# Optimization experiments

Measured on AMD Instinct MI355X. Metric: run time of the kernel, lower is better.

## Reference

```python
import jax, jax.numpy as jnp
import numpy as np

nT, nB, H, V = 256, 256, 1024, 32000

def setup_inputs() -> dict:
    key = jax.random.key(0)
    ks = jax.random.split(key, 16)
    s = 0.02
    return {
        "tokens": jax.random.randint(ks[0], (nB,), 0, V),
        "prev_hidden": jax.random.normal(ks[1], (1, nB, H), dtype=jnp.float32),
        "enc_outputs": jax.random.normal(ks[2], (nT, nB, H), dtype=jnp.float32),
        "emb": jax.random.normal(ks[3], (V, H), dtype=jnp.float32) * s,
        "W_i2h": jax.random.normal(ks[4], (H, H), dtype=jnp.float32) * s,
        "W_h2h": jax.random.normal(ks[5], (H, H), dtype=jnp.float32) * s,
        "b_h2h": jnp.zeros((H,), dtype=jnp.float32),
        "w_score": jax.random.normal(ks[6], (H,), dtype=jnp.float32) * s,
        "W_ih": jax.random.normal(ks[7], (3 * H, 2 * H), dtype=jnp.float32) * s,
        "b_ih": jnp.zeros((3 * H,), dtype=jnp.float32),
        "W_hh": jax.random.normal(ks[8], (3 * H, H), dtype=jnp.float32) * s,
        "b_hh": jnp.zeros((3 * H,), dtype=jnp.float32),
        "W_out": jax.random.normal(ks[9], (V, H), dtype=jnp.float32) * s,
        "b_out": jnp.zeros((V,), dtype=jnp.float32),
    }

def reference(tokens, prev_hidden, enc_outputs, emb, W_i2h, W_h2h, b_h2h,
              w_score, W_ih, b_ih, W_hh, b_hh, W_out, b_out):
    h0 = prev_hidden[0]                                     # [nB,H]
    cur_emb = emb[tokens]                                   # [nB,H] (dropout = identity at inference)
    # additive (Bahdanau) attention energies
    enc_proj = jnp.einsum('tbh,oh->tbo', enc_outputs, W_i2h)  # [nT,nB,H]
    h_proj = h0 @ W_h2h.T + b_h2h                           # [nB,H]
    e = jnp.einsum('tbh,h->tb', jnp.tanh(enc_proj + h_proj[None]), w_score)  # [nT,nB]
    alpha = jax.nn.softmax(e.T, axis=1)                     # [nB,nT], softmax over time
    context = jnp.einsum('bt,tbh->bh', alpha, enc_outputs)  # [nB,H]
    x = jnp.concatenate([context, cur_emb], axis=1)         # [nB,2H]
    # single GRU step (PyTorch gate order: r, z, n)
    gi = x @ W_ih.T + b_ih                                  # [nB,3H]
    gh = h0 @ W_hh.T + b_hh                                 # [nB,3H]
    hs = h0.shape[-1]
    r = jax.nn.sigmoid(gi[:, :hs] + gh[:, :hs])
    z = jax.nn.sigmoid(gi[:, hs:2*hs] + gh[:, hs:2*hs])
    n = jnp.tanh(gi[:, 2*hs:] + r * gh[:, 2*hs:])
    h_new = (1.0 - z) * n + z * h0                          # [nB,H]
    out = jax.nn.log_softmax(h_new @ W_out.T + b_out, axis=1)  # [nB,V]
    return out, h_new[None], alpha
```

## Files before the change

kernel.cpp:

```cpp
#include <hip/hip_runtime.h>
#include <hip/hip_bf16.h>

typedef __attribute__((ext_vector_type(8))) short bf16x8;
typedef __attribute__((ext_vector_type(4))) float f32x4;
typedef __attribute__((ext_vector_type(4))) int i32x4;
typedef __attribute__((ext_vector_type(4))) unsigned short u16x4;
typedef __attribute__((ext_vector_type(8))) unsigned short u16x8;

#define LDS_STRIDE 72

__device__ __forceinline__ unsigned short f2bf(float f) {
    __hip_bfloat16 h = __float2bfloat16(f);
    unsigned short u; __builtin_memcpy(&u, &h, 2); return u;
}
__device__ __forceinline__ float bf2f(unsigned short u) {
    union { unsigned u; float f; } v; v.u = ((unsigned)u) << 16; return v.f;
}
__device__ __forceinline__ float fast_sigmoid(float x) { return 1.f / (1.f + __expf(-x)); }
__device__ __forceinline__ float fast_tanh(float x)    { return 1.f - 2.f / (__expf(2.f * x) + 1.f); }

#define GLOAD_LDS16(gp, lp) __builtin_amdgcn_global_load_lds( \
    (const __attribute__((address_space(1))) void*)(gp), \
    (__attribute__((address_space(3))) void*)(lp), 16, 0, 0)


#define STA(LB, HF, PTR) do { \
    GLOAD_LDS16((PTR), &AL[LB][HF][ldsrow][0]); \
    GLOAD_LDS16((PTR) + 65536, &AL[LB][HF][64 + ldsrow][0]); \
} while (0)

#define STB(LB, HF, PTR) do { \
    GLOAD_LDS16((PTR), &BL[LB][HF][ldsrow][0]); \
    GLOAD_LDS16((PTR) + 65536, &BL[LB][HF][64 + ldsrow][0]); \
} while (0)

#define LDA(DST, BUF, MH, KS) do { \
    const int c_ = ((KS)*32 + fg*8) ^ swzr; \
    _Pragma("unroll") \
    for (int mi = 0; mi < 4; ++mi) \
        DST[mi] = *(const bf16x8*)&AL[BUF][wr][(MH)*64 + mi*16 + fr][c_]; \
} while (0)

#define LDB(DST, BUF, KS) do { \
    const int c_ = ((KS)*32 + fg*8) ^ swzr; \
    _Pragma("unroll") \
    for (int ni = 0; ni < 4; ++ni) \
        DST[ni] = *(const bf16x8*)&BL[BUF][bh][br0 + ni*16 + fr][c_]; \
} while (0)

#define MM(AV, BV, MH) do { \
    _Pragma("unroll") \
    for (int mi = 0; mi < 4; ++mi) \
        _Pragma("unroll") \
        for (int ni = 0; ni < 4; ++ni) \
            acc[(MH)*4 + mi][ni] = __builtin_amdgcn_mfma_f32_16x16x32_bf16( \
                AV[mi], BV[ni], acc[(MH)*4 + mi][ni], 0, 0, 0); \
} while (0)

#define SP1 __builtin_amdgcn_s_setprio(1)
#define SP0 __builtin_amdgcn_s_setprio(0)
#define BAR asm volatile("s_barrier" ::: "memory")
#define VMC8 asm volatile("s_waitcnt vmcnt(8)" ::: "memory")
#define VMC0 asm volatile("s_waitcnt vmcnt(0)" ::: "memory")

__global__ __launch_bounds__(512, 1)
void gemm8p_e(const unsigned short* __restrict__ Ag, const unsigned short* __restrict__ Bg,
              const float* __restrict__ hproj, const float* __restrict__ wscore,
              float* __restrict__ epart)
{
    const int tid = threadIdx.x;
    const int lane = tid & 63, wid = tid >> 6;
    const int fr = lane & 15, fg = lane >> 4;
    const int wr = wid >> 2;
    const int wc = wid & 3;
    const int bh = wc >> 1, br0 = (wc & 1) * 64;

    const int cpx = (int)gridDim.x >> 3;
    const int swz = ((int)blockIdx.x & 7) * cpx + ((int)blockIdx.x >> 3);
    const int mb = swz >> 2, nb = swz & 3;
    const int m0 = mb << 8, n0 = nb << 8;

    __shared__ unsigned short AL[3][2][128][64];
    __shared__ unsigned short BL[2][2][128][64];

    const int srow = lane >> 3;
    const int scol = ((lane & 7) ^ srow) << 3;
    const int swzr = (fr & 7) << 3;
    const int ldsrow = wid * 8;

    const unsigned short* pA0 = Ag + (size_t)(m0 + ldsrow + srow) * 1024 + scol;
    const unsigned short* pA1 = pA0 + (size_t)128 * 1024;
    const unsigned short* pB0 = Bg + (size_t)(n0 + ldsrow + srow) * 1024 + scol;
    const unsigned short* pB1 = pB0 + (size_t)128 * 1024;

    f32x4 acc[8][4];
#pragma unroll
    for (int i = 0; i < 8; ++i)
#pragma unroll
        for (int j = 0; j < 4; ++j) acc[i][j] = (f32x4){0.f, 0.f, 0.f, 0.f};
    bf16x8 avA[4], avB[4], bvA[4], bvB[4];

    STA(0, 0, pA0);      STA(0, 1, pA1);
    STB(0, 0, pB0);      STB(0, 1, pB1);
    STA(1, 0, pA0 + 64); STA(1, 1, pA1 + 64);
    STB(1, 0, pB0 + 64); STB(1, 1, pB1 + 64);
    VMC8;
    BAR;

#pragma unroll
    for (int t = 0; t < 16; t += 2) {
        const int tof = t * 64;
        const int a0 = t % 3, a1 = (t + 1) % 3, a2 = (t + 2) % 3, a3 = (t + 3) % 3;
        LDB(bvA, 0, 0); LDA(avA, a0, 0, 0);
        SP1; MM(avA, bvA, 0); SP0;
        LDB(bvB, 0, 1); LDA(avB, a0, 0, 1);
        if (t + 2 < 16) STA(a2, 0, pA0 + tof + 128);
        BAR;
        SP1; MM(avB, bvB, 0); SP0;
        LDA(avA, a0, 1, 0);
        if (t + 2 < 16) STA(a2, 1, pA1 + tof + 128);
        BAR;
        SP1; MM(avA, bvA, 1); SP0;
        LDA(avB, a0, 1, 1);
        if (t + 2 < 16) STB(0, 0, pB0 + tof + 128);
        BAR;
        SP1; MM(avB, bvB, 1); SP0;
        if (t + 2 < 16) { STB(0, 1, pB1 + tof + 128); VMC8; } else { VMC0; }
        BAR;
        LDB(bvA, 1, 0); LDA(avA, a1, 0, 0);
        SP1; MM(avA, bvA, 0); SP0;
        LDB(bvB, 1, 1); LDA(avB, a1, 0, 1);
        if (t + 3 < 16) STA(a3, 0, pA0 + tof + 192);
        BAR;
        SP1; MM(avB, bvB, 0); SP0;
        LDA(avA, a1, 1, 0);
        if (t + 3 < 16) STA(a3, 1, pA1 + tof + 192);
        BAR;
        SP1; MM(avA, bvA, 1); SP0;
        LDA(avB, a1, 1, 1);
        if (t + 3 < 16) STB(1, 0, pB0 + tof + 192);
        BAR;
        SP1; MM(avB, bvB, 1); SP0;
        if (t + 3 < 16) { STB(1, 1, pB1 + tof + 192); VMC8; }
        BAR;
    }

    float wsv[4];
#pragma unroll
    for (int ni = 0; ni < 4; ++ni) wsv[ni] = wscore[n0 + wc * 64 + ni * 16 + fr];
#pragma unroll
    for (int mi = 0; mi < 8; ++mi)
#pragma unroll
        for (int r = 0; r < 4; ++r) {
            const int bb = wr * 128 + mi * 16 + fg * 4 + r;
            const float* hp = hproj + (size_t)bb * 1024 + n0 + wc * 64 + fr;
            float s = 0.f;
#pragma unroll
            for (int ni = 0; ni < 4; ++ni)
                s += fast_tanh(acc[mi][ni][r] + hp[ni * 16]) * wsv[ni];
            s += __shfl_xor(s, 1); s += __shfl_xor(s, 2);
            s += __shfl_xor(s, 4); s += __shfl_xor(s, 8);
            if (fr == 0) epart[((size_t)bb * 256 + mb) * 16 + nb * 4 + wc] = s;
        }
}

__device__ void h2_body(char* smem, int blk, const float* __restrict__ h0,
                        const float* __restrict__ Wh2h, const float* __restrict__ Whh,
                        const float* __restrict__ bh2h, const float* __restrict__ bhh,
                        float* __restrict__ hproj, float* __restrict__ gh)
{
    const int mb = blk & 1;
    const int nbg = blk >> 1;
    const float* Bf; const float* bias; float* Cout; int Nst; int n0;
    if (nbg < 8) { Bf = Wh2h; bias = bh2h; Cout = hproj; Nst = 1024; n0 = nbg << 7; }
    else         { Bf = Whh;  bias = bhh;  Cout = gh;    Nst = 3072; n0 = (nbg - 8) << 7; }

    const int m0 = mb << 7;
    const int tid = threadIdx.x;
    const int lane = tid & 63, wid = tid >> 6;
    const int fr = lane & 15, fg = lane >> 4;
    const int srow = tid >> 1, shalf = (tid & 1) * 32;

    typedef unsigned short (*tile_t)[128][LDS_STRIDE];
    tile_t As = (tile_t)smem;
    tile_t Bs = (tile_t)(smem + 2 * 128 * LDS_STRIDE * 2);

    f32x4 acc[2][8];
#pragma unroll
    for (int i = 0; i < 2; ++i)
#pragma unroll
        for (int j = 0; j < 8; ++j) acc[i][j] = (f32x4){0.f, 0.f, 0.f, 0.f};

    float a_f[32], b_f[32];

    auto loadA = [&](int kt) {
        size_t base = (size_t)(m0 + srow) * 1024 + (size_t)kt * 64 + shalf;
#pragma unroll
        for (int j = 0; j < 8; ++j) *(f32x4*)&a_f[j * 4] = *(const f32x4*)(h0 + base + j * 4);
    };
    auto loadB = [&](int kt) {
        size_t base = (size_t)(n0 + srow) * 1024 + (size_t)kt * 64 + shalf;
#pragma unroll
        for (int j = 0; j < 8; ++j) *(f32x4*)&b_f[j * 4] = *(const f32x4*)(Bf + base + j * 4);
    };
    auto storeA = [&](int buf) {
        unsigned short t[32];
#pragma unroll
        for (int j = 0; j < 32; ++j) t[j] = f2bf(a_f[j]);
#pragma unroll
        for (int j = 0; j < 4; ++j) *(i32x4*)&As[buf][srow][shalf + j * 8] = *(i32x4*)&t[j * 8];
    };
    auto storeB = [&](int buf) {
        unsigned short t[32];
#pragma unroll
        for (int j = 0; j < 32; ++j) t[j] = f2bf(b_f[j]);
#pragma unroll
        for (int j = 0; j < 4; ++j) *(i32x4*)&Bs[buf][srow][shalf + j * 8] = *(i32x4*)&t[j * 8];
    };

    loadA(0); loadB(0);
    storeA(0); storeB(0);
    __syncthreads();

    for (int kt = 0; kt < 16; ++kt) {
        const int cur = kt & 1;
        if (kt + 1 < 16) { loadA(kt + 1); loadB(kt + 1); }
#pragma unroll
        for (int ks = 0; ks < 2; ++ks) {
            bf16x8 av[2], bv[8];
#pragma unroll
            for (int mi = 0; mi < 2; ++mi)
                av[mi] = *(const bf16x8*)&As[cur][wid * 32 + mi * 16 + fr][ks * 32 + fg * 8];
#pragma unroll
            for (int ni = 0; ni < 8; ++ni)
                bv[ni] = *(const bf16x8*)&Bs[cur][ni * 16 + fr][ks * 32 + fg * 8];
#pragma unroll
            for (int mi = 0; mi < 2; ++mi)
#pragma unroll
                for (int ni = 0; ni < 8; ++ni)
                    acc[mi][ni] = __builtin_amdgcn_mfma_f32_16x16x32_bf16(av[mi], bv[ni], acc[mi][ni], 0, 0, 0);
        }
        if (kt + 1 < 16) { storeA(cur ^ 1); storeB(cur ^ 1); }
        __syncthreads();
    }

#pragma unroll
    for (int mi = 0; mi < 2; ++mi)
#pragma unroll
        for (int r = 0; r < 4; ++r) {
            const int m = m0 + wid * 32 + mi * 16 + fg * 4 + r;
#pragma unroll
            for (int ni = 0; ni < 8; ++ni) {
                const int col = n0 + ni * 16 + fr;
                Cout[(size_t)m * Nst + col] = acc[mi][ni][r] + bias[col];
            }
        }
}

__global__ __launch_bounds__(256, 2)
void prep_h2(const float* __restrict__ enc, unsigned short* __restrict__ encB,
             const float* __restrict__ Wi2h, unsigned short* __restrict__ WiB,
             const float* __restrict__ emb, const int* __restrict__ tokens,
             unsigned short* __restrict__ xB,
             const float* __restrict__ h0,
             const float* __restrict__ Wh2h, const float* __restrict__ Whh,
             const float* __restrict__ bh2h, const float* __restrict__ bhh,
             float* __restrict__ hproj, float* __restrict__ gh)
{
    extern __shared__ char smem[];
    if (blockIdx.x < 64) {
        h2_body(smem, blockIdx.x, h0, Wh2h, Whh, bh2h, bhh, hproj, gh);
        return;
    }
    const int ENC4 = 16777216, WI4 = 262144, EMB4 = 65536;
    const int total = ENC4 + WI4 + EMB4;
    const int stride = ((int)gridDim.x - 64) * 256;
    for (int i = ((int)blockIdx.x - 64) * 256 + (int)threadIdx.x; i < total; i += stride) {
        f32x4 v; unsigned short* dst;
        if (i < ENC4) {
            v = *(const f32x4*)(enc + (size_t)i * 4);
            dst = encB + (size_t)i * 4;
        } else if (i < ENC4 + WI4) {
            int j = i - ENC4;
            v = *(const f32x4*)(Wi2h + (size_t)j * 4);
            dst = WiB + (size_t)j * 4;
        } else {
            int j = i - ENC4 - WI4;
            int b = j >> 8, h4 = j & 255;
            v = *(const f32x4*)(emb + (size_t)tokens[b] * 1024 + h4 * 4);
            dst = xB + (size_t)b * 2048 + 1024 + h4 * 4;
        }
        u16x4 o;
#pragma unroll
        for (int j = 0; j < 4; ++j) o[j] = f2bf(v[j]);
        *(u16x4*)dst = o;
    }
}

__global__ __launch_bounds__(256, 2)
void gemm_h2(const float* __restrict__ h0,
             const float* __restrict__ Wh2h, const float* __restrict__ Whh,
             const float* __restrict__ bh2h, const float* __restrict__ bhh,
             float* __restrict__ hproj, float* __restrict__ gh)
{
    extern __shared__ char smem[];
    h2_body(smem, blockIdx.x, h0, Wh2h, Whh, bh2h, bhh, hproj, gh);
}

__global__ __launch_bounds__(256) void sm_ctx(const float* __restrict__ epart,
                                              float* __restrict__ alpha,
                                              const unsigned short* __restrict__ encB,
                                              float* __restrict__ pc)
{
    const int b = blockIdx.x, tc = blockIdx.y;
    const int t = threadIdx.x;
    const int lane = t & 63, wv = t >> 6;

    const float* ep = epart + ((size_t)b * 256 + t) * 16;
    float s = 0.f;
#pragma unroll
    for (int j = 0; j < 16; ++j) s += ep[j];
    __shared__ float rmax[4], rsum[4];
    float mx = s;
#pragma unroll
    for (int d = 1; d < 64; d <<= 1) mx = fmaxf(mx, __shfl_xor(mx, d));
    if (lane == 0) rmax[wv] = mx;
    __syncthreads();
    mx = fmaxf(fmaxf(rmax[0], rmax[1]), fmaxf(rmax[2], rmax[3]));
    float p = __expf(s - mx);
    float sm = p;
#pragma unroll
    for (int d = 1; d < 64; d <<= 1) sm += __shfl_xor(sm, d);
    if (lane == 0) rsum[wv] = sm;
    __syncthreads();
    sm = rsum[0] + rsum[1] + rsum[2] + rsum[3];
    const float a = p / sm;
    if (tc == 0) alpha[(size_t)b * 256 + t] = a;

    __shared__ float al[256];
    al[t] = a;
    __syncthreads();

    if (t < 128) {
        const int h8 = t;
        float acc[8];
#pragma unroll
        for (int j = 0; j < 8; ++j) acc[j] = 0.f;
#pragma unroll 4
        for (int i = 0; i < 64; ++i) {
            const int tt = tc * 64 + i;
            const float av = al[tt];
            u16x8 e = *(const u16x8*)(encB + ((size_t)tt * 256 + b) * 1024 + h8 * 8);
#pragma unroll
            for (int j = 0; j < 8; ++j) acc[j] += bf2f(e[j]) * av;
        }
        float* d = pc + ((size_t)tc * 256 + b) * 1024 + h8 * 8;
        *(f32x4*)d = *(f32x4*)&acc[0];
        *(f32x4*)(d + 4) = *(f32x4*)&acc[4];
    }
}

__global__ __launch_bounds__(256, 2)
void gemm_gi(const unsigned short* __restrict__ xB, const float* __restrict__ Wih,
             float* __restrict__ gip)
{
    const int s = blockIdx.x / 48;
    const int blk = blockIdx.x % 48;
    const int mb = blk & 1, nb = blk >> 1;
    const int m0 = mb << 7, n0 = nb << 7;
    const int kbase = s * 256;
    const int tid = threadIdx.x;
    const int lane = tid & 63, wid = tid >> 6;
    const int fr = lane & 15, fg = lane >> 4;
    const int srow = tid >> 1, shalf = (tid & 1) * 32;

    extern __shared__ char smem[];
    typedef unsigned short (*tile_t)[128][LDS_STRIDE];
    tile_t As = (tile_t)smem;
    tile_t Bs = (tile_t)(smem + 2 * 128 * LDS_STRIDE * 2);

    f32x4 acc[2][8];
#pragma unroll
    for (int i = 0; i < 2; ++i)
#pragma unroll
        for (int j = 0; j < 8; ++j) acc[i][j] = (f32x4){0.f, 0.f, 0.f, 0.f};

    unsigned short a_b[32]; float b_f[32];

    auto loadA = [&](int kt) {
        size_t base = (size_t)(m0 + srow) * 2048 + kbase + (size_t)kt * 64 + shalf;
#pragma unroll
        for (int j = 0; j < 4; ++j) *(i32x4*)&a_b[j * 8] = *(const i32x4*)(xB + base + j * 8);
    };
    auto loadB = [&](int kt) {
        size_t base = (size_t)(n0 + srow) * 2048 + kbase + (size_t)kt * 64 + shalf;
#pragma unroll
        for (int j = 0; j < 8; ++j) *(f32x4*)&b_f[j * 4] = *(const f32x4*)(Wih + base + j * 4);
    };
    auto storeA = [&](int buf) {
#pragma unroll
        for (int j = 0; j < 4; ++j) *(i32x4*)&As[buf][srow][shalf + j * 8] = *(i32x4*)&a_b[j * 8];
    };
    auto storeB = [&](int buf) {
        unsigned short t[32];
#pragma unroll
        for (int j = 0; j < 32; ++j) t[j] = f2bf(b_f[j]);
#pragma unroll
        for (int j = 0; j < 4; ++j) *(i32x4*)&Bs[buf][srow][shalf + j * 8] = *(i32x4*)&t[j * 8];
    };

    loadA(0); loadB(0);
    storeA(0); storeB(0);
    __syncthreads();

    for (int kt = 0; kt < 4; ++kt) {
        const int cur = kt & 1;
        if (kt + 1 < 4) { loadA(kt + 1); loadB(kt + 1); }
#pragma unroll
        for (int ks = 0; ks < 2; ++ks) {
            bf16x8 av[2], bv[8];
#pragma unroll
            for (int mi = 0; mi < 2; ++mi)
                av[mi] = *(const bf16x8*)&As[cur][wid * 32 + mi * 16 + fr][ks * 32 + fg * 8];
#pragma unroll
            for (int ni = 0; ni < 8; ++ni)
                bv[ni] = *(const bf16x8*)&Bs[cur][ni * 16 + fr][ks * 32 + fg * 8];
#pragma unroll
            for (int mi = 0; mi < 2; ++mi)
#pragma unroll
                for (int ni = 0; ni < 8; ++ni)
                    acc[mi][ni] = __builtin_amdgcn_mfma_f32_16x16x32_bf16(av[mi], bv[ni], acc[mi][ni], 0, 0, 0);
        }
        if (kt + 1 < 4) { storeA(cur ^ 1); storeB(cur ^ 1); }
        __syncthreads();
    }

    float* Cs = gip + (size_t)s * 256 * 3072;
#pragma unroll
    for (int mi = 0; mi < 2; ++mi)
#pragma unroll
        for (int r = 0; r < 4; ++r) {
            const int m = m0 + wid * 32 + mi * 16 + fg * 4 + r;
#pragma unroll
            for (int ni = 0; ni < 8; ++ni) {
                const int col = n0 + ni * 16 + fr;
                Cs[(size_t)m * 3072 + col] = acc[mi][ni][r];
            }
        }
}

template<int EPI, bool ABF, bool BBF>
__global__ __launch_bounds__(256, 2)
void gemm_rs(const void* __restrict__ Agv, const void* __restrict__ Bgv,
             const float* __restrict__ bias, float* __restrict__ Cout,
             unsigned short* __restrict__ CoutB,
             const float* __restrict__ hproj, const float* __restrict__ wscore,
             float* __restrict__ epart, float* __restrict__ lsepart,
             int M, int N, int K)
{
    const int nbn = N >> 7;
    const int nmb = M >> 7;
    int mb, nb;
    if (EPI == 1) {
        int cpx = gridDim.x >> 3;
        int bp = (blockIdx.x & 7) * cpx + (blockIdx.x >> 3);
        mb = bp / nbn; nb = bp % nbn;
    } else {
        mb = blockIdx.x % nmb; nb = blockIdx.x / nmb;
    }
    const int m0 = mb << 7, n0 = nb << 7;
    const int tid = threadIdx.x;
    const int lane = tid & 63, wid = tid >> 6;
    const int fr = lane & 15, fg = lane >> 4;
    const int srow = tid >> 1, shalf = (tid & 1) * 32;

    extern __shared__ char smem[];
    typedef unsigned short (*tile_t)[128][LDS_STRIDE];
    tile_t As = (tile_t)smem;
    tile_t Bs = (tile_t)(smem + 2 * 128 * LDS_STRIDE * 2);

    const float* Af = (const float*)Agv;
    const unsigned short* Ab = (const unsigned short*)Agv;
    const float* Bf = (const float*)Bgv;
    const unsigned short* Bb = (const unsigned short*)Bgv;

    f32x4 acc[2][8];
#pragma unroll
    for (int i = 0; i < 2; ++i)
#pragma unroll
        for (int j = 0; j < 8; ++j) acc[i][j] = (f32x4){0.f, 0.f, 0.f, 0.f};

    float a_f[32]; unsigned short a_b[32];
    float b_f[32]; unsigned short b_b[32];

    auto loadA = [&](int kt) {
        size_t base = (size_t)(m0 + srow) * K + (size_t)kt * 64 + shalf;
        if (ABF) {
#pragma unroll
            for (int j = 0; j < 4; ++j) *(i32x4*)&a_b[j * 8] = *(const i32x4*)(Ab + base + j * 8);
        } else {
#pragma unroll
            for (int j = 0; j < 8; ++j) *(f32x4*)&a_f[j * 4] = *(const f32x4*)(Af + base + j * 4);
        }
    };
    auto loadB = [&](int kt) {
        size_t base = (size_t)(n0 + srow) * K + (size_t)kt * 64 + shalf;
        if (BBF) {
#pragma unroll
            for (int j = 0; j < 4; ++j) *(i32x4*)&b_b[j * 8] = *(const i32x4*)(Bb + base + j * 8);
        } else {
#pragma unroll
            for (int j = 0; j < 8; ++j) *(f32x4*)&b_f[j * 4] = *(const f32x4*)(Bf + base + j * 4);
        }
    };
    auto storeA = [&](int buf) {
        unsigned short tA[32];
        if (ABF) {
#pragma unroll
            for (int j = 0; j < 32; ++j) tA[j] = a_b[j];
        } else {
#pragma unroll
            for (int j = 0; j < 32; ++j) tA[j] = f2bf(a_f[j]);
        }
#pragma unroll
        for (int j = 0; j < 4; ++j) *(i32x4*)&As[buf][srow][shalf + j * 8] = *(i32x4*)&tA[j * 8];
    };
    auto storeB = [&](int buf) {
        unsigned short tB[32];
        if (BBF) {
#pragma unroll
            for (int j = 0; j < 32; ++j) tB[j] = b_b[j];
        } else {
#pragma unroll
            for (int j = 0; j < 32; ++j) tB[j] = f2bf(b_f[j]);
        }
#pragma unroll
        for (int j = 0; j < 4; ++j) *(i32x4*)&Bs[buf][srow][shalf + j * 8] = *(i32x4*)&tB[j * 8];
    };

    const int nkt = K >> 6;

    loadA(0); loadB(0);
    storeA(0); storeB(0);
    __syncthreads();

    for (int kt = 0; kt < nkt; ++kt) {
        const int cur = kt & 1;
        if (kt + 1 < nkt) { loadA(kt + 1); loadB(kt + 1); }
#pragma unroll
        for (int ks = 0; ks < 2; ++ks) {
            bf16x8 av[2], bv[8];
#pragma unroll
            for (int mi = 0; mi < 2; ++mi)
                av[mi] = *(const bf16x8*)&As[cur][wid * 32 + mi * 16 + fr][ks * 32 + fg * 8];
#pragma unroll
            for (int ni = 0; ni < 8; ++ni)
                bv[ni] = *(const bf16x8*)&Bs[cur][ni * 16 + fr][ks * 32 + fg * 8];
#pragma unroll
            for (int mi = 0; mi < 2; ++mi)
#pragma unroll
                for (int ni = 0; ni < 8; ++ni)
                    acc[mi][ni] = __builtin_amdgcn_mfma_f32_16x16x32_bf16(av[mi], bv[ni], acc[mi][ni], 0, 0, 0);
        }
        if (kt + 1 < nkt) { storeA(cur ^ 1); storeB(cur ^ 1); }
        __syncthreads();
    }

    if (EPI == 0) {
#pragma unroll
        for (int mi = 0; mi < 2; ++mi)
#pragma unroll
            for (int r = 0; r < 4; ++r) {
                const int m = m0 + wid * 32 + mi * 16 + fg * 4 + r;
#pragma unroll
                for (int ni = 0; ni < 8; ++ni) {
                    const int col = n0 + ni * 16 + fr;
                    Cout[(size_t)m * N + col] = acc[mi][ni][r] + bias[col];
                }
            }
    } else if (EPI == 1) {
        float wsv[8];
#pragma unroll
        for (int ni = 0; ni < 8; ++ni) wsv[ni] = wscore[n0 + ni * 16 + fr];
#pragma unroll
        for (int mi = 0; mi < 2; ++mi)
#pragma unroll
            for (int r = 0; r < 4; ++r) {
                const int m = m0 + wid * 32 + mi * 16 + fg * 4 + r;
                const int bb = m & 255, tt = m >> 8;
                const float* hp = hproj + (size_t)bb * 1024 + n0 + fr;
                float s = 0.f;
#pragma unroll
                for (int ni = 0; ni < 8; ++ni)
                    s += fast_tanh(acc[mi][ni][r] + hp[ni * 16]) * wsv[ni];
                s += __shfl_xor(s, 1); s += __shfl_xor(s, 2);
                s += __shfl_xor(s, 4); s += __shfl_xor(s, 8);
                if (fr == 0) epart[((size_t)bb * 256 + tt) * 8 + nb] = s;
            }
    } else {
#pragma unroll
        for (int mi = 0; mi < 2; ++mi)
#pragma unroll
            for (int r = 0; r < 4; ++r) {
                const int m = m0 + wid * 32 + mi * 16 + fg * 4 + r;
                float vv[8];
                float mx = -3.4e38f;
#pragma unroll
                for (int ni = 0; ni < 8; ++ni) {
                    const int col = n0 + ni * 16 + fr;
                    vv[ni] = acc[mi][ni][r] + bias[col];
                    CoutB[(size_t)m * N + col] = f2bf(vv[ni]);
                    mx = fmaxf(mx, vv[ni]);
                }
                mx = fmaxf(mx, __shfl_xor(mx, 1));
                mx = fmaxf(mx, __shfl_xor(mx, 2));
                mx = fmaxf(mx, __shfl_xor(mx, 4));
                mx = fmaxf(mx, __shfl_xor(mx, 8));
                float se = 0.f;
#pragma unroll
                for (int ni = 0; ni < 8; ++ni) se += __expf(vv[ni] - mx);
                se += __shfl_xor(se, 1); se += __shfl_xor(se, 2);
                se += __shfl_xor(se, 4); se += __shfl_xor(se, 8);
                if (fr == 0) {
                    lsepart[((size_t)m * nbn + nb) * 2]     = mx;
                    lsepart[((size_t)m * nbn + nb) * 2 + 1] = se;
                }
            }
    }
}

__global__ void prep_kernel(const float* __restrict__ Wi2h, unsigned short* __restrict__ WiB,
                            const float* __restrict__ emb, const int* __restrict__ tokens,
                            unsigned short* __restrict__ xB)
{
    int i = blockIdx.x * 256 + threadIdx.x;
    if (i < 262144) {
        f32x4 v = *(const f32x4*)(Wi2h + (size_t)i * 4);
        u16x4 o;
#pragma unroll
        for (int j = 0; j < 4; ++j) o[j] = f2bf(v[j]);
        *(u16x4*)(WiB + (size_t)i * 4) = o;
    } else {
        int j = i - 262144;
        int b = j >> 8, h4 = j & 255;
        int tok = tokens[b];
        f32x4 v = *(const f32x4*)(emb + (size_t)tok * 1024 + h4 * 4);
        u16x4 o;
#pragma unroll
        for (int jj = 0; jj < 4; ++jj) o[jj] = f2bf(v[jj]);
        *(u16x4*)(xB + (size_t)b * 2048 + 1024 + h4 * 4) = o;
    }
}

__global__ __launch_bounds__(256) void softmax_alpha(const float* __restrict__ epart,
                                                     float* __restrict__ alpha, int pw)
{
    const int b = blockIdx.x, t = threadIdx.x;
    const int lane = t & 63, w = t >> 6;
    const float* ep = epart + ((size_t)b * 256 + t) * pw;
    float s = 0.f;
    for (int j = 0; j < pw; ++j) s += ep[j];
    __shared__ float rmax[4], rsum[4];
    float mx = s;
#pragma unroll
    for (int d = 1; d < 64; d <<= 1) mx = fmaxf(mx, __shfl_xor(mx, d));
    if (lane == 0) rmax[w] = mx;
    __syncthreads();
    mx = fmaxf(fmaxf(rmax[0], rmax[1]), fmaxf(rmax[2], rmax[3]));
    float p = __expf(s - mx);
    float sm = p;
#pragma unroll
    for (int d = 1; d < 64; d <<= 1) sm += __shfl_xor(sm, d);
    if (lane == 0) rsum[w] = sm;
    __syncthreads();
    sm = rsum[0] + rsum[1] + rsum[2] + rsum[3];
    alpha[(size_t)b * 256 + t] = p / sm;
}

__global__ __launch_bounds__(256) void ctx_part(const float* __restrict__ alpha,
                                                const float* __restrict__ enc,
                                                float* __restrict__ pc)
{
    const int b = blockIdx.x, tc = blockIdx.y;
    const int h4 = threadIdx.x;
    const float* al = alpha + (size_t)b * 256 + tc * 64;
    f32x4 acc = {0.f, 0.f, 0.f, 0.f};
#pragma unroll 4
    for (int i = 0; i < 64; ++i) {
        float a = al[i];
        f32x4 e = *(const f32x4*)(enc + ((size_t)(tc * 64 + i) * 256 + b) * 1024 + h4 * 4);
        acc += e * a;
    }
    *(f32x4*)(pc + ((size_t)tc * 256 + b) * 1024 + h4 * 4) = acc;
}

__global__ void ctx_fin(const float* __restrict__ pc, unsigned short* __restrict__ xB)
{
    const int b = blockIdx.x, h4 = threadIdx.x;
    f32x4 c = {0.f, 0.f, 0.f, 0.f};
#pragma unroll
    for (int tc = 0; tc < 4; ++tc)
        c += *(const f32x4*)(pc + ((size_t)tc * 256 + b) * 1024 + h4 * 4);
    u16x4 o;
#pragma unroll
    for (int j = 0; j < 4; ++j) o[j] = f2bf(c[j]);
    *(u16x4*)(xB + (size_t)b * 2048 + h4 * 4) = o;
}

__global__ void gru8_kernel(const float* __restrict__ gip, const float* __restrict__ gh,
                            const float* __restrict__ bih, const float* __restrict__ h0,
                            float* __restrict__ hnew, unsigned short* __restrict__ hnB)
{
    int idx = blockIdx.x * 256 + threadIdx.x;
    int b = idx >> 10, h = idx & 1023;
    size_t gb = (size_t)b * 3072;
    const size_t S = (size_t)256 * 3072;
    float g0 = bih[h], g1 = bih[1024 + h], g2 = bih[2048 + h];
#pragma unroll
    for (int s = 0; s < 8; ++s) {
        g0 += gip[s * S + gb + h];
        g1 += gip[s * S + gb + 1024 + h];
        g2 += gip[s * S + gb + 2048 + h];
    }
    float r = fast_sigmoid(g0 + gh[gb + h]);
    float z = fast_sigmoid(g1 + gh[gb + 1024 + h]);
    float n = fast_tanh   (g2 + r * gh[gb + 2048 + h]);
    float hp = h0[idx];
    float hn = (1.f - z) * n + z * hp;
    hnew[idx] = hn;
    hnB[idx] = f2bf(hn);
}

__global__ void gru_kernel(const float* __restrict__ gi, const float* __restrict__ gh,
                           const float* __restrict__ h0, float* __restrict__ hnew,
                           unsigned short* __restrict__ hnB)
{
    int idx = blockIdx.x * 256 + threadIdx.x;
    int b = idx >> 10, h = idx & 1023;
    size_t gb = (size_t)b * 3072;
    float r = fast_sigmoid(gi[gb + h]        + gh[gb + h]);
    float z = fast_sigmoid(gi[gb + 1024 + h] + gh[gb + 1024 + h]);
    float n = fast_tanh   (gi[gb + 2048 + h] + r * gh[gb + 2048 + h]);
    float hp = h0[idx];
    float hn = (1.f - z) * n + z * hp;
    hnew[idx] = hn;
    hnB[idx] = f2bf(hn);
}

__global__ __launch_bounds__(256) void lse_sub(const float* __restrict__ lsepart,
                                               const unsigned short* __restrict__ lgB,
                                               float* __restrict__ out)
{
    const int m = blockIdx.x, tid = threadIdx.x;
    const int lane = tid & 63, w = tid >> 6;
    float mx = -3.4e38f, s = 0.f;
    if (tid < 250) {
        mx = lsepart[((size_t)m * 250 + tid) * 2];
        s  = lsepart[((size_t)m * 250 + tid) * 2 + 1];
    }
#pragma unroll
    for (int d = 1; d < 64; d <<= 1) {
        float om = __shfl_xor(mx, d), os = __shfl_xor(s, d);
        float nm = fmaxf(mx, om);
        s = s * __expf(mx - nm) + os * __expf(om - nm);
        mx = nm;
    }
    __shared__ float smx[4], ssm[4];
    if (lane == 0) { smx[w] = mx; ssm[w] = s; }
    __syncthreads();
    float fm = smx[0], fs = ssm[0];
#pragma unroll
    for (int i = 1; i < 4; ++i) {
        float nm = fmaxf(fm, smx[i]);
        fs = fs * __expf(fm - nm) + ssm[i] * __expf(smx[i] - nm);
        fm = nm;
    }
    const float lse = fm + __logf(fs);
    const unsigned short* lrow = lgB + (size_t)m * 32000;
    float* orow = out + (size_t)m * 32000;
    for (int j = tid; j < 4000; j += 256) {
        u16x8 v = *(const u16x8*)(lrow + (size_t)j * 8);
        f32x4 o0, o1;
#pragma unroll
        for (int k = 0; k < 4; ++k) o0[k] = bf2f(v[k]) - lse;
#pragma unroll
        for (int k = 0; k < 4; ++k) o1[k] = bf2f(v[4 + k]) - lse;
        *(f32x4*)(orow + (size_t)j * 8) = o0;
        *(f32x4*)(orow + (size_t)j * 8 + 4) = o1;
    }
}

__global__ void lse_reduce(const float* __restrict__ lsepart, float* __restrict__ lse, int nbn)
{
    const int m = blockIdx.x, l = threadIdx.x;
    float mx = -3.4e38f, s = 0.f;
    for (int p = l; p < nbn; p += 64) {
        float pm = lsepart[((size_t)m * nbn + p) * 2];
        float ps = lsepart[((size_t)m * nbn + p) * 2 + 1];
        float nm = fmaxf(mx, pm);
        s = s * __expf(mx - nm) + ps * __expf(pm - nm);
        mx = nm;
    }
#pragma unroll
    for (int d = 1; d < 64; d <<= 1) {
        float om = __shfl_xor(mx, d), os = __shfl_xor(s, d);
        float nm = fmaxf(mx, om);
        s = s * __expf(mx - nm) + os * __expf(om - nm);
        mx = nm;
    }
    if (l == 0) lse[m] = mx + __logf(s);
}

__global__ void lsub_bf(const unsigned short* __restrict__ lgB,
                        const float* __restrict__ lse, float* __restrict__ out)
{
    int f = blockIdx.x * 256 + threadIdx.x;
    float l = lse[f / 4000];
    u16x8 v = *(const u16x8*)(lgB + (size_t)f * 8);
    float* o = out + (size_t)f * 8;
    f32x4 o0, o1;
#pragma unroll
    for (int j = 0; j < 4; ++j) o0[j] = bf2f(v[j]) - l;
#pragma unroll
    for (int j = 0; j < 4; ++j) o1[j] = bf2f(v[4 + j]) - l;
    *(f32x4*)o = o0;
    *(f32x4*)(o + 4) = o1;
}

extern "C" void kernel_launch(void* const* d_in, const int* in_sizes, int n_in,
                              void* d_out, int out_size, void* d_ws, size_t ws_size,
                              hipStream_t stream)
{
    const int*   tokens  = (const int*)  d_in[0];
    const float* h0      = (const float*)d_in[1];
    const float* enc     = (const float*)d_in[2];
    const float* emb     = (const float*)d_in[3];
    const float* W_i2h   = (const float*)d_in[4];
    const float* W_h2h   = (const float*)d_in[5];
    const float* b_h2h   = (const float*)d_in[6];
    const float* w_score = (const float*)d_in[7];
    const float* W_ih    = (const float*)d_in[8];
    const float* b_ih    = (const float*)d_in[9];
    const float* W_hh    = (const float*)d_in[10];
    const float* b_hh    = (const float*)d_in[11];
    const float* W_out   = (const float*)d_in[12];
    const float* b_out   = (const float*)d_in[13];

    float* out   = (float*)d_out;
    float* hnew  = out + (size_t)256 * 32000;
    float* alpha = hnew + 256 * 1024;

    const size_t RS_LDS = 2u * 2u * 128u * LDS_STRIDE * 2u;

    char* w = (char*)d_ws;
    const size_t NEED = (size_t)153 * (1 << 20);

    if (ws_size >= NEED) {
        unsigned short* encB  = (unsigned short*)(w);
        unsigned short* lgB   = (unsigned short*)(w);
        float* gip            = (float*)(w + (size_t)32 * (1 << 20));
        unsigned short* WiB   = (unsigned short*)(w + (size_t)128 * (1 << 20));
        float* hproj          = (float*)(w + (size_t)130 * (1 << 20));
        float* gh             = (float*)(w + (size_t)131 * (1 << 20));
        float* epart          = (float*)(w + (size_t)134 * (1 << 20));
        float* pc             = (float*)(w + (size_t)138 * (1 << 20));
        unsigned short* xB    = (unsigned short*)(w + (size_t)142 * (1 << 20));
        unsigned short* hnB   = (unsigned short*)(w + (size_t)150 * (1 << 20));
        float* lsepart        = (float*)(w + (size_t)151 * (1 << 20));

        prep_h2<<<2112, 256, RS_LDS, stream>>>(enc, encB, W_i2h, WiB, emb, tokens, xB,
                                               h0, W_h2h, W_hh, b_h2h, b_hh, hproj, gh);
        gemm8p_e<<<1024, 512, 0, stream>>>(encB, WiB, hproj, w_score, epart);
        sm_ctx<<<dim3(256, 4), 256, 0, stream>>>(epart, alpha, encB, pc);
        ctx_fin<<<256, 256, 0, stream>>>(pc, xB);
        gemm_gi<<<384, 256, RS_LDS, stream>>>(xB, W_ih, gip);
        gru8_kernel<<<1024, 256, 0, stream>>>(gip, gh, b_ih, h0, hnew, hnB);
        gemm_rs<2, true, false><<<500, 256, RS_LDS, stream>>>(hnB, W_out, b_out, nullptr,
            lgB, nullptr, nullptr, nullptr, lsepart, 256, 32000, 1024);
        lse_sub<<<256, 256, 0, stream>>>(lsepart, lgB, out);
    } else {
        unsigned short* WiB   = (unsigned short*)(w);
        float* hproj          = (float*)(w + (size_t)2  * (1 << 20));
        float* gh             = (float*)(w + (size_t)3  * (1 << 20));
        float* epart          = (float*)(w + (size_t)6  * (1 << 20));
        float* pc             = (float*)(w + (size_t)8  * (1 << 20));
        unsigned short* xB    = (unsigned short*)(w + (size_t)12 * (1 << 20));
        float* gi             = (float*)(w + (size_t)13 * (1 << 20));
        unsigned short* hnB   = (unsigned short*)(w + (size_t)16 * (1 << 20));
        float* lsepart        = (float*)(w + (size_t)17 * (1 << 20));
        float* lse            = (float*)(w + (size_t)18 * (1 << 20));
        unsigned short* lgB   = (unsigned short*)(w + (size_t)19 * (1 << 20));

        prep_kernel<<<1280, 256, 0, stream>>>(W_i2h, WiB, emb, tokens, xB);
        gemm_h2<<<64, 256, RS_LDS, stream>>>(h0, W_h2h, W_hh, b_h2h, b_hh, hproj, gh);
        gemm_rs<1, false, true><<<4096, 256, RS_LDS, stream>>>(enc, WiB, nullptr, nullptr,
            nullptr, hproj, w_score, epart, nullptr, 65536, 1024, 1024);
        softmax_alpha<<<256, 256, 0, stream>>>(epart, alpha, 8);
        ctx_part<<<dim3(256, 4), 256, 0, stream>>>(alpha, enc, pc);
        ctx_fin<<<256, 256, 0, stream>>>(pc, xB);
        gemm_rs<0, true, false><<<48, 256, RS_LDS, stream>>>(xB, W_ih, b_ih, gi,
            nullptr, nullptr, nullptr, nullptr, nullptr, 256, 3072, 2048);
        gru_kernel<<<1024, 256, 0, stream>>>(gi, gh, h0, hnew, hnB);
        gemm_rs<2, true, false><<<500, 256, RS_LDS, stream>>>(hnB, W_out, b_out, nullptr,
            lgB, nullptr, nullptr, nullptr, lsepart, 256, 32000, 1024);
        lse_reduce<<<256, 64, 0, stream>>>(lsepart, lse, 250);
        lsub_bf<<<4000, 256, 0, stream>>>(lgB, lse, out);
    }
}
```

Measured before the change: 413.5 us.

## Add full-M output-projection GEMM so each block reads W_out once

Replaces the 500-block output-projection GEMM with a 250-block kernel where each block covers all 256 batch rows and 128 vocab columns. Each slice of W_out is then converted and staged once rather than once per M-half, which cuts redundant fp32 weight traffic. A is staged through global-load-to-LDS with a swizzle, and B is register-prefetched one k-step ahead. The fallback path also swaps lse_reduce plus lsub_bf for the fused lse_sub with a partition count argument. The cost is fewer blocks (250 on a 256-CU part) and heavier per-block register use with launch bounds capping occupancy at one block.

```diff
diff --git a/kernel.cpp b/kernel.cpp
--- a/kernel.cpp
+++ b/kernel.cpp
@@ -164,6 +164,111 @@
         }
 }
 
+__global__ __launch_bounds__(256, 1)
+void gemm_lg(const unsigned short* __restrict__ A, const float* __restrict__ Bf,
+             const float* __restrict__ bias, unsigned short* __restrict__ lgB,
+             float* __restrict__ lsepart)
+{
+    const int nb = blockIdx.x;
+    const int n0 = nb << 7;
+    const int tid = threadIdx.x;
+    const int lane = tid & 63, wid = tid >> 6;
+    const int fr = lane & 15, fg = lane >> 4;
+    const int wr = wid >> 1, wc = wid & 1;
+
+    __shared__ unsigned short ALg[2][256][64];
+    __shared__ unsigned short Bsg[2][128][LDS_STRIDE];
+
+    const int srow8 = lane >> 3;
+    const int scol = ((lane & 7) ^ srow8) << 3;
+    const int swzr = (fr & 7) << 3;
+    const int srow = tid >> 1, shalf = (tid & 1) * 32;
+
+    f32x4 acc[8][4];
+#pragma unroll
+    for (int i = 0; i < 8; ++i)
+#pragma unroll
+        for (int j = 0; j < 4; ++j) acc[i][j] = (f32x4){0.f, 0.f, 0.f, 0.f};
+
+    float b_f[32];
+
+    auto stageA = [&](int buf, int kt) {
+        const size_t kof = (size_t)kt * 64 + scol;
+#pragma unroll
+        for (int i = 0; i < 8; ++i) {
+            const int row = i * 32 + wid * 8;
+            GLOAD_LDS16(A + (size_t)(row + srow8) * 1024 + kof, &ALg[buf][row][0]);
+        }
+    };
+    auto loadB = [&](int kt) {
+        size_t base = (size_t)(n0 + srow) * 1024 + (size_t)kt * 64 + shalf;
+#pragma unroll
+        for (int j = 0; j < 8; ++j) *(f32x4*)&b_f[j * 4] = *(const f32x4*)(Bf + base + j * 4);
+    };
+    auto storeB = [&](int buf) {
+        unsigned short t[32];
+#pragma unroll
+        for (int j = 0; j < 32; ++j) t[j] = f2bf(b_f[j]);
+#pragma unroll
+        for (int j = 0; j < 4; ++j) *(i32x4*)&Bsg[buf][srow][shalf + j * 8] = *(i32x4*)&t[j * 8];
+    };
+
+    loadB(0); stageA(0, 0); storeB(0);
+    __syncthreads();
+
+    for (int kt = 0; kt < 16; ++kt) {
+        const int cur = kt & 1;
+        if (kt + 1 < 16) { loadB(kt + 1); stageA(cur ^ 1, kt + 1); }
+#pragma unroll
+        for (int ks = 0; ks < 2; ++ks) {
+            const int col = (ks * 32 + fg * 8) ^ swzr;
+            bf16x8 av[8], bv[4];
+#pragma unroll
+            for (int mi = 0; mi < 8; ++mi)
+                av[mi] = *(const bf16x8*)&ALg[cur][wr * 128 + mi * 16 + fr][col];
+#pragma unroll
+            for (int ni = 0; ni < 4; ++ni)
+                bv[ni] = *(const bf16x8*)&Bsg[cur][wc * 64 + ni * 16 + fr][ks * 32 + fg * 8];
+#pragma unroll
+            for (int mi = 0; mi < 8; ++mi)
+#pragma unroll
+                for (int ni = 0; ni < 4; ++ni)
+                    acc[mi][ni] = __builtin_amdgcn_mfma_f32_16x16x32_bf16(av[mi], bv[ni], acc[mi][ni], 0, 0, 0);
+        }
+        if (kt + 1 < 16) storeB(cur ^ 1);
+        __syncthreads();
+    }
+
+#pragma unroll
+    for (int mi = 0; mi < 8; ++mi)
+#pragma unroll
+        for (int r = 0; r < 4; ++r) {
+            const int m = wr * 128 + mi * 16 + fg * 4 + r;
+            float vv[4];
+            float mx = -3.4e38f;
+#pragma unroll
+            for (int ni = 0; ni < 4; ++ni) {
+                const int colg = n0 + wc * 64 + ni * 16 + fr;
+                vv[ni] = acc[mi][ni][r] + bias[colg];
+                lgB[(size_t)m * 32000 + colg] = f2bf(vv[ni]);
+                mx = fmaxf(mx, vv[ni]);
+            }
+            mx = fmaxf(mx, __shfl_xor(mx, 1));
+            mx = fmaxf(mx, __shfl_xor(mx, 2));
+            mx = fmaxf(mx, __shfl_xor(mx, 4));
+            mx = fmaxf(mx, __shfl_xor(mx, 8));
+            float se = 0.f;
+#pragma unroll
+            for (int ni = 0; ni < 4; ++ni) se += __expf(vv[ni] - mx);
+            se += __shfl_xor(se, 1); se += __shfl_xor(se, 2);
+            se += __shfl_xor(se, 4); se += __shfl_xor(se, 8);
+            if (fr == 0) {
+                lsepart[((size_t)m * 500 + nb * 2 + wc) * 2]     = mx;
+                lsepart[((size_t)m * 500 + nb * 2 + wc) * 2 + 1] = se;
+            }
+        }
+}
+
 __device__ void h2_body(char* smem, int blk, const float* __restrict__ h0,
                         const float* __restrict__ Wh2h, const float* __restrict__ Whh,
                         const float* __restrict__ bh2h, const float* __restrict__ bhh,
@@ -749,14 +854,17 @@
 
 __global__ __launch_bounds__(256) void lse_sub(const float* __restrict__ lsepart,
                                                const unsigned short* __restrict__ lgB,
-                                               float* __restrict__ out)
+                                               float* __restrict__ out, int np)
 {
     const int m = blockIdx.x, tid = threadIdx.x;
     const int lane = tid & 63, w = tid >> 6;
     float mx = -3.4e38f, s = 0.f;
-    if (tid < 250) {
-        mx = lsepart[((size_t)m * 250 + tid) * 2];
-        s  = lsepart[((size_t)m * 250 + tid) * 2 + 1];
+    for (int p = tid; p < np; p += 256) {
+        float pm = lsepart[((size_t)m * np + p) * 2];
+        float ps = lsepart[((size_t)m * np + p) * 2 + 1];
+        float nm = fmaxf(mx, pm);
+        s = s * __expf(mx - nm) + ps * __expf(pm - nm);
+        mx = nm;
     }
 #pragma unroll
     for (int d = 1; d < 64; d <<= 1) {
@@ -788,43 +896,6 @@
         *(f32x4*)(orow + (size_t)j * 8) = o0;
         *(f32x4*)(orow + (size_t)j * 8 + 4) = o1;
     }
-}
-
-__global__ void lse_reduce(const float* __restrict__ lsepart, float* __restrict__ lse, int nbn)
-{
-    const int m = blockIdx.x, l = threadIdx.x;
-    float mx = -3.4e38f, s = 0.f;
-    for (int p = l; p < nbn; p += 64) {
-        float pm = lsepart[((size_t)m * nbn + p) * 2];
-        float ps = lsepart[((size_t)m * nbn + p) * 2 + 1];
-        float nm = fmaxf(mx, pm);
-        s = s * __expf(mx - nm) + ps * __expf(pm - nm);
-        mx = nm;
-    }
-#pragma unroll
-    for (int d = 1; d < 64; d <<= 1) {
-        float om = __shfl_xor(mx, d), os = __shfl_xor(s, d);
-        float nm = fmaxf(mx, om);
-        s = s * __expf(mx - nm) + os * __expf(om - nm);
-        mx = nm;
-    }
-    if (l == 0) lse[m] = mx + __logf(s);
-}
-
-__global__ void lsub_bf(const unsigned short* __restrict__ lgB,
-                        const float* __restrict__ lse, float* __restrict__ out)
-{
-    int f = blockIdx.x * 256 + threadIdx.x;
-    float l = lse[f / 4000];
-    u16x8 v = *(const u16x8*)(lgB + (size_t)f * 8);
-    float* o = out + (size_t)f * 8;
-    f32x4 o0, o1;
-#pragma unroll
-    for (int j = 0; j < 4; ++j) o0[j] = bf2f(v[j]) - l;
-#pragma unroll
-    for (int j = 0; j < 4; ++j) o1[j] = bf2f(v[4 + j]) - l;
-    *(f32x4*)o = o0;
-    *(f32x4*)(o + 4) = o1;
 }
 
 extern "C" void kernel_launch(void* const* d_in, const int* in_sizes, int n_in,
@@ -875,9 +946,8 @@
         ctx_fin<<<256, 256, 0, stream>>>(pc, xB);
         gemm_gi<<<384, 256, RS_LDS, stream>>>(xB, W_ih, gip);
         gru8_kernel<<<1024, 256, 0, stream>>>(gip, gh, b_ih, h0, hnew, hnB);
-        gemm_rs<2, true, false><<<500, 256, RS_LDS, stream>>>(hnB, W_out, b_out, nullptr,
-            lgB, nullptr, nullptr, nullptr, lsepart, 256, 32000, 1024);
-        lse_sub<<<256, 256, 0, stream>>>(lsepart, lgB, out);
+        gemm_lg<<<250, 256, 0, stream>>>(hnB, W_out, b_out, lgB, lsepart);
+        lse_sub<<<256, 256, 0, stream>>>(lsepart, lgB, out, 500);
     } else {
         unsigned short* WiB   = (unsigned short*)(w);
         float* hproj          = (float*)(w + (size_t)2  * (1 << 20));
@@ -888,7 +958,6 @@
         float* gi             = (float*)(w + (size_t)13 * (1 << 20));
         unsigned short* hnB   = (unsigned short*)(w + (size_t)16 * (1 << 20));
         float* lsepart        = (float*)(w + (size_t)17 * (1 << 20));
-        float* lse            = (float*)(w + (size_t)18 * (1 << 20));
         unsigned short* lgB   = (unsigned short*)(w + (size_t)19 * (1 << 20));
 
         prep_kernel<<<1280, 256, 0, stream>>>(W_i2h, WiB, emb, tokens, xB);
@@ -903,7 +972,6 @@
         gru_kernel<<<1024, 256, 0, stream>>>(gi, gh, h0, hnew, hnB);
         gemm_rs<2, true, false><<<500, 256, RS_LDS, stream>>>(hnB, W_out, b_out, nullptr,
             lgB, nullptr, nullptr, nullptr, lsepart, 256, 32000, 1024);
-        lse_reduce<<<256, 64, 0, stream>>>(lsepart, lse, 250);
-        lsub_bf<<<4000, 256, 0, stream>>>(lgB, lse, out);
-    }
-}
+        lse_sub<<<256, 256, 0, stream>>>(lsepart, lgB, out, 250);
+    }
+}
```

Result: no change. 415.9 us (+0.6%).
